# Optimization experiments

Hardware: AMD Instinct MI355X
Metric: run time of the kernel (lower is better)

Reference implementation:

```python
import jax, jax.numpy as jnp
import numpy as np
import math

N_FUNC = 32
LR_START, LR_DECAY = 1.0, 0.977
WEIGHT_DECAY, AMP_DECAY, MM_LR = 0.01, 0.01, 0.03
N_SAMP, BATCH, MOMENTUM = 32, 16, 0.85
N_FEAT, N_TARGET, MEM_SIZE = 1024, 512, 16384
DATA_SIZE = 100
SQRT_NF = math.sqrt(N_FUNC)


def setup_inputs() -> dict:
    key = jax.random.key(0)
    ks = jax.random.split(key, 16)
    p = jnp.linspace(0.01, 0.99, N_FUNC)[:, None]
    center_freq = jnp.log(p / (1.0 - p))  # logit of linspace, as in __init__
    return {
        "t": DATA_SIZE,
        "data_size": DATA_SIZE,
        "ts": jax.random.randint(ks[0], (N_SAMP,), 0, DATA_SIZE + 1),
        "x": jax.random.normal(ks[1], (N_FEAT,), jnp.float32),
        "z": jax.random.normal(ks[2], (N_TARGET,), jnp.float32),
        "memory": jax.random.normal(ks[3], (MEM_SIZE, N_TARGET), jnp.float32),
        "t_memory": jax.random.randint(ks[4], (MEM_SIZE,), 0, DATA_SIZE),
        "feat_memory": jax.random.normal(ks[5], (MEM_SIZE, N_FEAT), jnp.float32),
        "amp_re": 1.0 / SQRT_NF + 0.01 * jax.random.normal(ks[6], (N_FUNC, N_TARGET), jnp.float32),
        "amp_im": 0.01 * jax.random.normal(ks[7], (N_FUNC, N_TARGET), jnp.float32),
        "freq": 0.1 * jax.random.normal(ks[8], (N_FUNC, 1), jnp.float32),
        "center_freq": center_freq.astype(jnp.float32),
        "res_proj": 0.02 * jax.random.normal(ks[9], (N_FEAT + N_TARGET, N_TARGET), jnp.float32),
        "feat_mean": 0.1 * jax.random.normal(ks[10], (N_FEAT,), jnp.float32),
        "bias": 0.1 * jax.random.normal(ks[11], (N_TARGET,), jnp.float32),
        "amp_grad_re": 0.01 * jax.random.normal(ks[12], (N_FUNC, N_TARGET), jnp.float32),
        "amp_grad_im": 0.01 * jax.random.normal(ks[13], (N_FUNC, N_TARGET), jnp.float32),
        "freq_grad": 0.01 * jax.random.normal(ks[14], (N_FUNC, 1), jnp.float32),
        "res_proj_grad": 0.001 * jax.random.normal(ks[15], (N_FEAT + N_TARGET, N_TARGET), jnp.float32),
    }


def _get_freq(freq, center_freq):
    fr = center_freq + jnp.tanh(freq) * (64.0 / N_FUNC)
    return jax.nn.sigmoid(fr) * 0.5


def _evaluate(t, amp_re, amp_im, freq, bias, center_freq):
    # t: [B]; amp: [F, T]; freq/center_freq: [F, 1]
    fr = _get_freq(freq, center_freq)                      # [F, 1]
    ph = (2.0 * math.pi) * t[:, None, None] * fr           # [B, F, 1]
    # Re(exp(i*ph) * (amp_re + i*amp_im)) = cos*amp_re - sin*amp_im
    z = (jnp.cos(ph) * amp_re - jnp.sin(ph) * amp_im).sum(1) / SQRT_NF
    return z + bias                                        # [B, T]


def _get_resid(x, z, res_proj, feat_mean, bias):
    r = jnp.concatenate([x - feat_mean, z - bias], axis=-1) @ res_proj
    return r / (jnp.abs(r) + 1.0)


def reference(t, data_size, ts, x, z, memory, t_memory, feat_memory,
              amp_re, amp_im, freq, center_freq, res_proj, feat_mean, bias,
              amp_grad_re, amp_grad_im, freq_grad, res_proj_grad):
    # scatter new sample into the ring buffers
    memory = memory.at[data_size].set(z)
    feat_memory = feat_memory.at[data_size].set(x)
    t_memory = t_memory.at[data_size].set(t)
    ds_new = data_size + 1
    lr = LR_START * LR_DECAY ** ds_new  # lr after this call's decay
    # running means (torch uses the already-incremented data_size)
    bias = (bias * ds_new + z) / (ds_new + 1)
    feat_mean = (feat_mean * ds_new + x) / (ds_new + 1)

    for b in range(N_SAMP // BATCH):
        batch = ts[b * BATCH:(b + 1) * BATCH]
        t_b = t_memory[batch].astype(jnp.float32)
        z_b = memory[batch]
        x_b = feat_memory[batch]

        def loss_fn(a_re, a_im, fq, rp):
            z_ = _evaluate(t_b, a_re, a_im, fq, bias, center_freq)
            amp_abs = jnp.sqrt(a_re ** 2 + a_im ** 2)
            loss = jnp.sqrt(amp_abs).sum() * AMP_DECAY
            loss = loss + jnp.abs(z_b - z_).sum(-1).mean()
            resid = _get_resid(x_b, z_, rp, feat_mean, bias)
            z2 = jax.lax.stop_gradient(z_) + resid
            res_loss = jnp.abs(z_b - z2).sum(-1).mean()
            # torch uses self.res_proj (buffer) here -> no grad through this term
            res_loss = res_loss + jnp.abs(jax.lax.stop_gradient(rp)).sum() * WEIGHT_DECAY
            return loss + res_loss * MM_LR

        ag_re, ag_im, fg, rg = jax.grad(loss_fn, argnums=(0, 1, 2, 3))(amp_re, amp_im, freq, res_proj)
        # momentum decay then normalized-grad accumulate, then SGD step
        anorm = jnp.sqrt((ag_re ** 2).sum() + (ag_im ** 2).sum()) + 1.0  # complex vector norm
        amp_grad_re = amp_grad_re * MOMENTUM + ag_re / anorm
        amp_grad_im = amp_grad_im * MOMENTUM + ag_im / anorm
        amp_re = amp_re - amp_grad_re * lr
        amp_im = amp_im - amp_grad_im * lr
        fnorm = jnp.sqrt((fg ** 2).sum()) + 1.0
        freq_grad = freq_grad * MOMENTUM + fg / fnorm
        freq = freq - freq_grad * lr
        rnorm = jnp.sqrt((rg ** 2).sum()) + 1.0
        res_proj_grad = res_proj_grad * MOMENTUM + rg / rnorm
        res_proj = res_proj - res_proj_grad * lr

    return (memory, t_memory, feat_memory, amp_re, amp_im, freq, res_proj,
            bias, feat_mean, amp_grad_re, amp_grad_im, freq_grad, res_proj_grad)
```

## Files before the change

kernel.cpp:

```cpp
#include <hip/hip_runtime.h>
#include <math.h>

#define NT 512
#define NF 1024
#define NFUNC 32
#define BATCHSZ 16

constexpr int O_MEM  = 0;
constexpr int O_TMEM = 8388608;
constexpr int O_FEAT = 8404992;
constexpr int O_ARE  = 25182208;
constexpr int O_AIM  = 25198592;
constexpr int O_FREQ = 25214976;
constexpr int O_RP   = 25215008;
constexpr int O_BIAS = 26001440;
constexpr int O_FM   = 26001952;
constexpr int O_AGR  = 26002976;
constexpr int O_AGI  = 26019360;
constexpr int O_FGR  = 26035744;
constexpr int O_RPG  = 26035776;

constexpr int W_LR    = 0;
constexpr int W_ANORM = 2;
constexpr int W_RNORM = 4;
constexpr int W_GFR   = 8;
constexpr int W_TB    = 72;
constexpr int W_C     = 96;
constexpr int W_S     = 608;
constexpr int W_CATZ  = 1120;
constexpr int W_CATX  = 9312;
constexpr int W_GR    = 25696;
constexpr int W_G     = 33888;
constexpr int W_AGRE  = 42080;
constexpr int W_AGIM  = 58464;
constexpr int W_RPART = 74848;

constexpr float MM_LR = 0.03f;
constexpr float AMP_DECAY = 0.01f;
constexpr float MOM = 0.85f;
constexpr float INV_SQRT_NF = 0.17677669529663687f;
constexpr float TWO_PI = 6.283185307179586f;

constexpr int NCOPY = 192;
constexpr long long U_TOTAL = 6295552LL;

__device__ __forceinline__ float sgnf(float x) {
    return (x > 0.f) ? 1.f : ((x < 0.f) ? -1.f : 0.f);
}

__device__ __forceinline__ float wave_reduce(float v) {
#pragma unroll
    for (int o = 32; o > 0; o >>= 1) v += __shfl_down(v, o, 64);
    return v;
}

__device__ __forceinline__ void copy_role(int rb, int cbase, int ccnt,
    const int* __restrict__ tptr, const int* __restrict__ dsptr,
    const float* __restrict__ x, const float* __restrict__ z,
    const float* __restrict__ memory, const int* __restrict__ t_memory,
    const float* __restrict__ feat_memory, float* __restrict__ out)
{
    const int dsv = *dsptr;
    const int tt  = *tptr;
    const int nthr = NCOPY * 256;
    for (int q = rb * 256 + (int)threadIdx.x; q * 4 < ccnt; q += nthr) {
#pragma unroll
        for (int w = 0; w < 4; ++w) {
            int rel = q * 4 + w;
            if (rel >= ccnt) break;
            int u = cbase + rel;
            if (u < 2097152) {
                int row = u >> 7;
                float4 v = (row == dsv) ? ((const float4*)z)[u & 127]
                                        : ((const float4*)memory)[u];
                ((float4*)(out + O_MEM))[u] = v;
            } else if (u < 6291456) {
                int f = u - 2097152;
                int row = f >> 8;
                float4 v = (row == dsv) ? ((const float4*)x)[f & 255]
                                        : ((const float4*)feat_memory)[f];
                ((float4*)(out + O_FEAT))[f] = v;
            } else {
                int f = u - 6291456;
                int4 iv = ((const int4*)t_memory)[f];
                int e = f * 4;
                float* o = out + O_TMEM + e;
                o[0] = (e + 0 == dsv) ? (float)tt : (float)iv.x;
                o[1] = (e + 1 == dsv) ? (float)tt : (float)iv.y;
                o[2] = (e + 2 == dsv) ? (float)tt : (float)iv.z;
                o[3] = (e + 3 == dsv) ? (float)tt : (float)iv.w;
            }
        }
    }
}

#define COPY_ARGS const int* __restrict__ tptr, const int* __restrict__ dsptr,            \
                  const float* __restrict__ x, const float* __restrict__ z,               \
                  const float* __restrict__ memory, const int* __restrict__ t_memory,     \
                  const float* __restrict__ feat_memory, int cbase, int ccnt
#define COPY_PASS tptr, dsptr, x, z, memory, t_memory, feat_memory

__global__ __launch_bounds__(256) void k_fwd_a(int b, const int* __restrict__ ts,
    const float* __restrict__ cf,
    const float* __restrict__ are_src, const float* __restrict__ aim_src,
    const float* __restrict__ fq_src, const float* __restrict__ fm_in,
    float* __restrict__ out, float* __restrict__ ws, COPY_ARGS)
{
    const int bb = blockIdx.x, tid = threadIdx.x;
    if (bb >= 16) { copy_role(bb - 16, cbase, ccnt, COPY_PASS, out); return; }
    __shared__ float c_l[32], s_l[32];
    const int i = bb;
    const int dsv = *dsptr;
    const int bi = ts[b * BATCHSZ + i];
    if (tid < 32) {
        float f  = fq_src[tid];
        float th = tanhf(f);
        float u  = cf[tid] + 2.f * th;
        float sg = 1.f / (1.f + expf(-u));
        float fr = 0.5f * sg;
        float tb = (bi == dsv) ? (float)(*tptr) : (float)t_memory[bi];
        float ph = TWO_PI * tb * fr;
        float cv = cosf(ph), sv = sinf(ph);
        c_l[tid] = cv; s_l[tid] = sv;
        ws[W_C + i*32 + tid] = cv; ws[W_S + i*32 + tid] = sv;
        if (tid == 0) ws[W_TB + i] = tb;
    }
    if (i == 0) {
        if (tid == 64) ws[W_ANORM + b] = 0.f;
        if (tid == 65) ws[W_RNORM + b] = 0.f;
        if (tid == 66 && b == 0) ws[W_LR] = (float)pow(0.977, (double)(dsv + 1));
        if (tid >= 96 && tid < 128) ws[W_GFR + b*32 + tid - 96] = 0.f;
    }
    __syncthreads();
#pragma unroll
    for (int qq = 0; qq < 2; ++qq) {
        int q = tid + qq * 256;
        float acc = 0.f;
#pragma unroll
        for (int k = 0; k < 32; ++k)
            acc += c_l[k] * are_src[k*NT + q] - s_l[k] * aim_src[k*NT + q];
        ws[W_CATZ + i*NT + q] = acc * INV_SQRT_NF;
    }
    const float nn = (float)(dsv + 1), dd = (float)(dsv + 2);
#pragma unroll
    for (int pp = 0; pp < 4; ++pp) {
        int p = tid + pp * 256;
        float fmv = (fm_in[p] * nn + x[p]) / dd;
        float xv  = (bi == dsv) ? x[p] : feat_memory[bi*NF + p];
        ws[W_CATX + i*NF + p] = xv - fmv;
    }
}

__global__ __launch_bounds__(256) void k_fwd_b(const float* __restrict__ rp_src,
    float* __restrict__ out, float* __restrict__ ws, COPY_ARGS)
{
    const int bb = blockIdx.x, tid = threadIdx.x;
    if (bb >= 256) { copy_role(bb - 256, cbase, ccnt, COPY_PASS, out); return; }
    const int i = bb >> 4, s = bb & 15;
    __shared__ float cat[96];
    if (tid < 96) {
        int p = s * 96 + tid;
        cat[tid] = (p < NF) ? ws[W_CATX + i*NF + p] : ws[W_CATZ + i*NT + p - NF];
    }
    __syncthreads();
    const int j = tid;
    const float* rpb = rp_src + (size_t)s * 96 * NT;
    float a0 = 0.f, a1 = 0.f, b0 = 0.f, b1 = 0.f;
#pragma unroll 8
    for (int p = 0; p < 96; p += 2) {
        float c0 = cat[p], c1 = cat[p + 1];
        a0 += c0 * rpb[p*NT + j];
        a1 += c0 * rpb[p*NT + j + 256];
        b0 += c1 * rpb[(p+1)*NT + j];
        b1 += c1 * rpb[(p+1)*NT + j + 256];
    }
    ws[W_RPART + s*8192 + i*NT + j]       = a0 + b0;
    ws[W_RPART + s*8192 + i*NT + j + 256] = a1 + b1;
}

__global__ __launch_bounds__(256) void k_eplg(int b, const int* __restrict__ ts,
    const float* __restrict__ bias_in, const float* __restrict__ fm_in,
    float* __restrict__ out, float* __restrict__ ws, COPY_ARGS)
{
    const int bb = blockIdx.x, tid = threadIdx.x;
    if (bb >= 32) { copy_role(bb - 32, cbase, ccnt, COPY_PASS, out); return; }
    const int e = bb * 256 + tid;
    const int i = e >> 9, j = e & 511;
    const int dsv = *dsptr;
    float r = 0.f;
#pragma unroll
    for (int s = 0; s < 16; ++s) r += ws[W_RPART + s*8192 + e];
    const float nn = (float)(dsv + 1), dd = (float)(dsv + 2);
    float bn = (bias_in[j] * nn + z[j]) / dd;
    float zj = ws[W_CATZ + e] + bn;
    const int bi = ts[b * BATCHSZ + i];
    float zb = (bi == dsv) ? z[j] : memory[bi*NT + j];
    float s1 = sgnf(zj - zb);
    float ar = fabsf(r) + 1.f;
    float z2 = zj + r / ar;
    float g  = sgnf(z2 - zb) * (MM_LR / 16.f) / (ar * ar);
    ws[W_GR + e] = g;
    ws[W_G  + e] = s1 * (1.f / 16.f);
    if (b == 0) {
        if (e < 512)  out[O_BIAS + e] = bn;
        if (e < 1024) out[O_FM + e] = (fm_in[e] * nn + x[e]) / dd;
    }
}

__global__ __launch_bounds__(256) void k_gr(int b, const float* __restrict__ rp_src,
    float* __restrict__ out, float* __restrict__ ws, COPY_ARGS)
{
    __shared__ float red[4];
    const int bb = blockIdx.x, tid = threadIdx.x;
    if (bb >= 5120) { copy_role(bb - 5120, cbase, ccnt, COPY_PASS, out); return; }
    if (bb < 2048) {
        int wid = tid >> 6, lane = tid & 63;
        int e = bb*4 + wid;
        int i = e >> 9, j = e & 511;
        const float* grow = ws + W_GR + i*NT;
        const float* rrow = rp_src + (size_t)(NF + j) * NT;
        float acc = 0.f;
#pragma unroll
        for (int l = lane; l < NT; l += 64) acc += grow[l] * rrow[l];
        acc = wave_reduce(acc);
        if (lane == 0) ws[W_G + e] += acc;
    } else {
        int e = (bb - 2048)*256 + tid;
        int p = e >> 9, j = e & 511;
        float rg = 0.f;
#pragma unroll
        for (int i2 = 0; i2 < 16; ++i2) {
            float cat = (p < NF) ? ws[W_CATX + i2*NF + p]
                                 : ws[W_CATZ + i2*NT + (p - NF)];
            rg += cat * ws[W_GR + i2*NT + j];
        }
        float v = wave_reduce(rg * rg);
        if ((tid & 63) == 0) red[tid >> 6] = v;
        __syncthreads();
        if (tid == 0) atomicAdd(&ws[W_RNORM + b], red[0]+red[1]+red[2]+red[3]);
    }
}

__global__ __launch_bounds__(256) void k_ag(int b,
    const float* __restrict__ are_src, const float* __restrict__ aim_src,
    float* __restrict__ out, float* __restrict__ ws, COPY_ARGS)
{
    __shared__ float red[4];
    const int bb = blockIdx.x, tid = threadIdx.x;
    if (bb >= 192) { copy_role(bb - 192, cbase, ccnt, COPY_PASS, out); return; }
    if (bb < 64) {
        int e = bb*256 + tid;
        int k = e >> 9;
        float gre = 0.f, gim = 0.f;
#pragma unroll
        for (int i2 = 0; i2 < 16; ++i2) {
            float G = ws[W_G + i2*NT + (e & 511)];
            gre += G * ws[W_C + i2*32 + k];
            gim += G * ws[W_S + i2*32 + k];
        }
        float re = are_src[e], im = aim_src[e];
        float aa = sqrtf(re*re + im*im);
        float dec = AMP_DECAY / (2.f * aa * sqrtf(aa));
        float agr =  gre * INV_SQRT_NF + re * dec;
        float agi = -gim * INV_SQRT_NF + im * dec;
        ws[W_AGRE + e] = agr;
        ws[W_AGIM + e] = agi;
        float v = wave_reduce(agr*agr + agi*agi);
        if ((tid & 63) == 0) red[tid >> 6] = v;
        __syncthreads();
        if (tid == 0) atomicAdd(&ws[W_ANORM + b], red[0]+red[1]+red[2]+red[3]);
    } else {
        int wid = tid >> 6, lane = tid & 63;
        int pair = (bb - 64)*4 + wid;
        int i = pair >> 5, k = pair & 31;
        float ck = ws[W_C + i*32 + k], sk = ws[W_S + i*32 + k];
        float acc = 0.f;
#pragma unroll
        for (int j = lane; j < NT; j += 64)
            acc += ws[W_G + i*NT + j] * (-sk * are_src[k*NT + j] - ck * aim_src[k*NT + j]);
        acc = wave_reduce(acc);
        if (lane == 0)
            atomicAdd(&ws[W_GFR + b*32 + k], acc * TWO_PI * ws[W_TB + i] * INV_SQRT_NF);
    }
}

__global__ __launch_bounds__(256) void k_upd(int b, const float* __restrict__ cf,
    const float* __restrict__ are_src, const float* __restrict__ aim_src,
    const float* __restrict__ agr_src, const float* __restrict__ agi_src,
    const float* __restrict__ fq_src,  const float* __restrict__ fgr_src,
    const float* __restrict__ rp_src,  const float* __restrict__ rpg_src,
    float* __restrict__ out, float* __restrict__ ws, COPY_ARGS)
{
    const int bb = blockIdx.x, tid = threadIdx.x;
    if (bb >= 3137) { copy_role(bb - 3137, cbase, ccnt, COPY_PASS, out); return; }
    const float lr = ws[W_LR];
    if (bb < 64) {
        int e = bb*256 + tid;
        float anorm = sqrtf(ws[W_ANORM + b]) + 1.f;
        float mr = agr_src[e]*MOM + ws[W_AGRE + e]/anorm;
        out[O_AGR + e] = mr; out[O_ARE + e] = are_src[e] - mr*lr;
        float mi = agi_src[e]*MOM + ws[W_AGIM + e]/anorm;
        out[O_AGI + e] = mi; out[O_AIM + e] = aim_src[e] - mi*lr;
    } else if (bb == 64) {
        if (tid < 64) {
            float fg = 0.f, th = 0.f;
            if (tid < 32) {
                float f = fq_src[tid];
                th = tanhf(f);
                float u  = cf[tid] + 2.f*th;
                float sg = 1.f / (1.f + expf(-u));
                fg = ws[W_GFR + b*32 + tid] * sg*(1.f-sg)*(1.f-th*th);
            }
            float t2 = fg*fg;
#pragma unroll
            for (int o = 32; o > 0; o >>= 1) t2 += __shfl_down(t2, o, 64);
            float tot = __shfl(t2, 0, 64);
            if (tid < 32) {
                float fnorm = sqrtf(tot) + 1.f;
                float m = fgr_src[tid]*MOM + fg/fnorm;
                out[O_FGR + tid] = m;
                out[O_FREQ + tid] = fq_src[tid] - m*lr;
            }
        }
    } else {
        int e = (bb - 65)*256 + tid;
        int p = e >> 9, j = e & 511;
        float rg = 0.f;
#pragma unroll
        for (int i2 = 0; i2 < 16; ++i2) {
            float cat = (p < NF) ? ws[W_CATX + i2*NF + p]
                                 : ws[W_CATZ + i2*NT + (p - NF)];
            rg += cat * ws[W_GR + i2*NT + j];
        }
        float rnorm = sqrtf(ws[W_RNORM + b]) + 1.f;
        float m = rpg_src[e]*MOM + rg/rnorm;
        out[O_RPG + e] = m; out[O_RP + e] = rp_src[e] - m*lr;
    }
}

extern "C" void kernel_launch(void* const* d_in, const int* in_sizes, int n_in,
                              void* d_out, int out_size, void* d_ws, size_t ws_size,
                              hipStream_t stream)
{
    const int*   t            = (const int*)d_in[0];
    const int*   dsp          = (const int*)d_in[1];
    const int*   ts           = (const int*)d_in[2];
    const float* x            = (const float*)d_in[3];
    const float* z            = (const float*)d_in[4];
    const float* memory       = (const float*)d_in[5];
    const int*   t_memory     = (const int*)d_in[6];
    const float* feat_memory  = (const float*)d_in[7];
    const float* amp_re       = (const float*)d_in[8];
    const float* amp_im       = (const float*)d_in[9];
    const float* freq         = (const float*)d_in[10];
    const float* cf           = (const float*)d_in[11];
    const float* res_proj     = (const float*)d_in[12];
    const float* feat_mean    = (const float*)d_in[13];
    const float* bias         = (const float*)d_in[14];
    const float* amp_grad_re  = (const float*)d_in[15];
    const float* amp_grad_im  = (const float*)d_in[16];
    const float* freq_grad    = (const float*)d_in[17];
    const float* res_proj_grad= (const float*)d_in[18];
    float* out = (float*)d_out;
    float* ws  = (float*)d_ws;

    const float* ARE[2] = { amp_re,        out + O_ARE };
    const float* AIM[2] = { amp_im,        out + O_AIM };
    const float* AGR[2] = { amp_grad_re,   out + O_AGR };
    const float* AGI[2] = { amp_grad_im,   out + O_AGI };
    const float* FQ [2] = { freq,          out + O_FREQ };
    const float* FGR[2] = { freq_grad,     out + O_FGR };
    const float* RP [2] = { res_proj,      out + O_RP };
    const float* RPG[2] = { res_proj_grad, out + O_RPG };

    const int per = 524628;
    int base = 0, k = 0;
    auto nxt = [&](int& cb, int& cc) {
        cb = base;
        cc = (k == 11) ? (int)(U_TOTAL - base) : per;
        base += cc; ++k;
    };
    int cb, cc;
    for (int b = 0; b < 2; ++b) {
        nxt(cb, cc);
        k_fwd_a<<<16 + NCOPY, 256, 0, stream>>>(b, ts, cf, ARE[b], AIM[b], FQ[b],
            feat_mean, out, ws, t, dsp, x, z, memory, t_memory, feat_memory, cb, cc);
        nxt(cb, cc);
        k_fwd_b<<<256 + NCOPY, 256, 0, stream>>>(RP[b], out, ws,
            t, dsp, x, z, memory, t_memory, feat_memory, cb, cc);
        nxt(cb, cc);
        k_eplg<<<32 + NCOPY, 256, 0, stream>>>(b, ts, bias, feat_mean, out, ws,
            t, dsp, x, z, memory, t_memory, feat_memory, cb, cc);
        nxt(cb, cc);
        k_gr<<<5120 + NCOPY, 256, 0, stream>>>(b, RP[b], out, ws,
            t, dsp, x, z, memory, t_memory, feat_memory, cb, cc);
        nxt(cb, cc);
        k_ag<<<192 + NCOPY, 256, 0, stream>>>(b, ARE[b], AIM[b], out, ws,
            t, dsp, x, z, memory, t_memory, feat_memory, cb, cc);
        nxt(cb, cc);
        k_upd<<<3137 + NCOPY, 256, 0, stream>>>(b, cf, ARE[b], AIM[b], AGR[b], AGI[b],
            FQ[b], FGR[b], RP[b], RPG[b], out, ws,
            t, dsp, x, z, memory, t_memory, feat_memory, cb, cc);
    }
}
```

Measured before the change: 376.9 us.

## Fuse forward stages and gradient matvec, cutting per-step kernel launches

```diff
diff --git a/kernel.cpp b/kernel.cpp
--- a/kernel.cpp
+++ b/kernel.cpp
@@ -41,7 +41,7 @@
 constexpr float INV_SQRT_NF = 0.17677669529663687f;
 constexpr float TWO_PI = 6.283185307179586f;
 
-constexpr int NCOPY = 192;
+constexpr int NCOPY = 256;
 constexpr long long U_TOTAL = 6295552LL;
 
 __device__ __forceinline__ float sgnf(float x) {
@@ -100,16 +100,17 @@
                   const float* __restrict__ feat_memory, int cbase, int ccnt
 #define COPY_PASS tptr, dsptr, x, z, memory, t_memory, feat_memory
 
-__global__ __launch_bounds__(256) void k_fwd_a(int b, const int* __restrict__ ts,
+__global__ __launch_bounds__(256) void k_fwd_ab(int b, const int* __restrict__ ts,
     const float* __restrict__ cf,
     const float* __restrict__ are_src, const float* __restrict__ aim_src,
     const float* __restrict__ fq_src, const float* __restrict__ fm_in,
+    const float* __restrict__ rp_src,
     float* __restrict__ out, float* __restrict__ ws, COPY_ARGS)
 {
     const int bb = blockIdx.x, tid = threadIdx.x;
-    if (bb >= 16) { copy_role(bb - 16, cbase, ccnt, COPY_PASS, out); return; }
-    __shared__ float c_l[32], s_l[32];
-    const int i = bb;
+    if (bb >= 256) { copy_role(bb - 256, cbase, ccnt, COPY_PASS, out); return; }
+    const int i = bb >> 4, s = bb & 15;
+    __shared__ float c_l[32], s_l[32], cat[96];
     const int dsv = *dsptr;
     const int bi = ts[b * BATCHSZ + i];
     if (tid < 32) {
@@ -122,45 +123,37 @@
         float ph = TWO_PI * tb * fr;
         float cv = cosf(ph), sv = sinf(ph);
         c_l[tid] = cv; s_l[tid] = sv;
-        ws[W_C + i*32 + tid] = cv; ws[W_S + i*32 + tid] = sv;
-        if (tid == 0) ws[W_TB + i] = tb;
-    }
-    if (i == 0) {
+        if (s == 0) {
+            ws[W_C + i*32 + tid] = cv; ws[W_S + i*32 + tid] = sv;
+            if (tid == 0) ws[W_TB + i] = tb;
+        }
+    }
+    if (bb == 0) {
         if (tid == 64) ws[W_ANORM + b] = 0.f;
         if (tid == 65) ws[W_RNORM + b] = 0.f;
         if (tid == 66 && b == 0) ws[W_LR] = (float)pow(0.977, (double)(dsv + 1));
         if (tid >= 96 && tid < 128) ws[W_GFR + b*32 + tid - 96] = 0.f;
     }
     __syncthreads();
-#pragma unroll
-    for (int qq = 0; qq < 2; ++qq) {
-        int q = tid + qq * 256;
-        float acc = 0.f;
-#pragma unroll
-        for (int k = 0; k < 32; ++k)
-            acc += c_l[k] * are_src[k*NT + q] - s_l[k] * aim_src[k*NT + q];
-        ws[W_CATZ + i*NT + q] = acc * INV_SQRT_NF;
-    }
-    const float nn = (float)(dsv + 1), dd = (float)(dsv + 2);
-#pragma unroll
-    for (int pp = 0; pp < 4; ++pp) {
-        int p = tid + pp * 256;
-        float fmv = (fm_in[p] * nn + x[p]) / dd;
-        float xv  = (bi == dsv) ? x[p] : feat_memory[bi*NF + p];
-        ws[W_CATX + i*NF + p] = xv - fmv;
-    }
-}
-
-__global__ __launch_bounds__(256) void k_fwd_b(const float* __restrict__ rp_src,
-    float* __restrict__ out, float* __restrict__ ws, COPY_ARGS)
-{
-    const int bb = blockIdx.x, tid = threadIdx.x;
-    if (bb >= 256) { copy_role(bb - 256, cbase, ccnt, COPY_PASS, out); return; }
-    const int i = bb >> 4, s = bb & 15;
-    __shared__ float cat[96];
     if (tid < 96) {
         int p = s * 96 + tid;
-        cat[tid] = (p < NF) ? ws[W_CATX + i*NF + p] : ws[W_CATZ + i*NT + p - NF];
+        float cv;
+        if (p < NF) {
+            const float nn = (float)(dsv + 1), dd = (float)(dsv + 2);
+            float fmv = (fm_in[p] * nn + x[p]) / dd;
+            float xv  = (bi == dsv) ? x[p] : feat_memory[bi*NF + p];
+            cv = xv - fmv;
+            ws[W_CATX + i*NF + p] = cv;
+        } else {
+            int q = p - NF;
+            float acc = 0.f;
+#pragma unroll
+            for (int k = 0; k < 32; ++k)
+                acc += c_l[k] * are_src[k*NT + q] - s_l[k] * aim_src[k*NT + q];
+            cv = acc * INV_SQRT_NF;
+            ws[W_CATZ + i*NT + q] = cv;
+        }
+        cat[tid] = cv;
     }
     __syncthreads();
     const int j = tid;
@@ -178,76 +171,63 @@
     ws[W_RPART + s*8192 + i*NT + j + 256] = a1 + b1;
 }
 
-__global__ __launch_bounds__(256) void k_eplg(int b, const int* __restrict__ ts,
+__global__ __launch_bounds__(256) void k_eplg2(int b, const int* __restrict__ ts,
     const float* __restrict__ bias_in, const float* __restrict__ fm_in,
+    const float* __restrict__ rp_src,
     float* __restrict__ out, float* __restrict__ ws, COPY_ARGS)
 {
     const int bb = blockIdx.x, tid = threadIdx.x;
     if (bb >= 32) { copy_role(bb - 32, cbase, ccnt, COPY_PASS, out); return; }
-    const int e = bb * 256 + tid;
-    const int i = e >> 9, j = e & 511;
+    const int i = bb >> 1, half = bb & 1;
+    __shared__ float g_sh[NT], d_sh[NT];
     const int dsv = *dsptr;
-    float r = 0.f;
-#pragma unroll
-    for (int s = 0; s < 16; ++s) r += ws[W_RPART + s*8192 + e];
+    const int bi = ts[b * BATCHSZ + i];
     const float nn = (float)(dsv + 1), dd = (float)(dsv + 2);
-    float bn = (bias_in[j] * nn + z[j]) / dd;
-    float zj = ws[W_CATZ + e] + bn;
-    const int bi = ts[b * BATCHSZ + i];
-    float zb = (bi == dsv) ? z[j] : memory[bi*NT + j];
-    float s1 = sgnf(zj - zb);
-    float ar = fabsf(r) + 1.f;
-    float z2 = zj + r / ar;
-    float g  = sgnf(z2 - zb) * (MM_LR / 16.f) / (ar * ar);
-    ws[W_GR + e] = g;
-    ws[W_G  + e] = s1 * (1.f / 16.f);
-    if (b == 0) {
-        if (e < 512)  out[O_BIAS + e] = bn;
-        if (e < 1024) out[O_FM + e] = (fm_in[e] * nn + x[e]) / dd;
-    }
-}
-
-__global__ __launch_bounds__(256) void k_gr(int b, const float* __restrict__ rp_src,
+#pragma unroll
+    for (int ll = 0; ll < 2; ++ll) {
+        int l = tid + ll * 256;
+        float r = 0.f;
+#pragma unroll
+        for (int s = 0; s < 16; ++s) r += ws[W_RPART + s*8192 + i*NT + l];
+        float bn = (bias_in[l] * nn + z[l]) / dd;
+        float zj = ws[W_CATZ + i*NT + l] + bn;
+        float zb = (bi == dsv) ? z[l] : memory[bi*NT + l];
+        float s1 = sgnf(zj - zb);
+        float ar = fabsf(r) + 1.f;
+        float z2 = zj + r / ar;
+        float g  = sgnf(z2 - zb) * (MM_LR / 16.f) / (ar * ar);
+        g_sh[l] = g; d_sh[l] = s1 * (1.f / 16.f);
+        ws[W_GR + i*NT + l] = g;
+        if (b == 0 && bb == 0) out[O_BIAS + l] = bn;
+    }
+    if (b == 0 && bb < 2) {
+#pragma unroll
+        for (int ll = 0; ll < 2; ++ll) {
+            int p = half * 512 + tid + ll * 256;
+            out[O_FM + p] = (fm_in[p] * nn + x[p]) / dd;
+        }
+    }
+    __syncthreads();
+    const int w = tid >> 6, lane = tid & 63;
+    const int jbase = half * 256 + w * 64;
+    for (int jj = 0; jj < 64; ++jj) {
+        int j = jbase + jj;
+        const float* rrow = rp_src + (size_t)(NF + j) * NT;
+        float acc = 0.f;
+#pragma unroll
+        for (int l = lane; l < NT; l += 64) acc += g_sh[l] * rrow[l];
+        acc = wave_reduce(acc);
+        if (lane == 0) ws[W_G + i*NT + j] = d_sh[j] + acc;
+    }
+}
+
+__global__ __launch_bounds__(256) void k_norms(int b,
+    const float* __restrict__ are_src, const float* __restrict__ aim_src,
     float* __restrict__ out, float* __restrict__ ws, COPY_ARGS)
 {
     __shared__ float red[4];
     const int bb = blockIdx.x, tid = threadIdx.x;
-    if (bb >= 5120) { copy_role(bb - 5120, cbase, ccnt, COPY_PASS, out); return; }
-    if (bb < 2048) {
-        int wid = tid >> 6, lane = tid & 63;
-        int e = bb*4 + wid;
-        int i = e >> 9, j = e & 511;
-        const float* grow = ws + W_GR + i*NT;
-        const float* rrow = rp_src + (size_t)(NF + j) * NT;
-        float acc = 0.f;
-#pragma unroll
-        for (int l = lane; l < NT; l += 64) acc += grow[l] * rrow[l];
-        acc = wave_reduce(acc);
-        if (lane == 0) ws[W_G + e] += acc;
-    } else {
-        int e = (bb - 2048)*256 + tid;
-        int p = e >> 9, j = e & 511;
-        float rg = 0.f;
-#pragma unroll
-        for (int i2 = 0; i2 < 16; ++i2) {
-            float cat = (p < NF) ? ws[W_CATX + i2*NF + p]
-                                 : ws[W_CATZ + i2*NT + (p - NF)];
-            rg += cat * ws[W_GR + i2*NT + j];
-        }
-        float v = wave_reduce(rg * rg);
-        if ((tid & 63) == 0) red[tid >> 6] = v;
-        __syncthreads();
-        if (tid == 0) atomicAdd(&ws[W_RNORM + b], red[0]+red[1]+red[2]+red[3]);
-    }
-}
-
-__global__ __launch_bounds__(256) void k_ag(int b,
-    const float* __restrict__ are_src, const float* __restrict__ aim_src,
-    float* __restrict__ out, float* __restrict__ ws, COPY_ARGS)
-{
-    __shared__ float red[4];
-    const int bb = blockIdx.x, tid = threadIdx.x;
-    if (bb >= 192) { copy_role(bb - 192, cbase, ccnt, COPY_PASS, out); return; }
+    if (bb >= 3264) { copy_role(bb - 3264, cbase, ccnt, COPY_PASS, out); return; }
     if (bb < 64) {
         int e = bb*256 + tid;
         int k = e >> 9;
@@ -269,7 +249,7 @@
         if ((tid & 63) == 0) red[tid >> 6] = v;
         __syncthreads();
         if (tid == 0) atomicAdd(&ws[W_ANORM + b], red[0]+red[1]+red[2]+red[3]);
-    } else {
+    } else if (bb < 192) {
         int wid = tid >> 6, lane = tid & 63;
         int pair = (bb - 64)*4 + wid;
         int i = pair >> 5, k = pair & 31;
@@ -281,6 +261,20 @@
         acc = wave_reduce(acc);
         if (lane == 0)
             atomicAdd(&ws[W_GFR + b*32 + k], acc * TWO_PI * ws[W_TB + i] * INV_SQRT_NF);
+    } else {
+        int e = (bb - 192)*256 + tid;
+        int p = e >> 9, j = e & 511;
+        float rg = 0.f;
+#pragma unroll
+        for (int i2 = 0; i2 < 16; ++i2) {
+            float cat = (p < NF) ? ws[W_CATX + i2*NF + p]
+                                 : ws[W_CATZ + i2*NT + (p - NF)];
+            rg += cat * ws[W_GR + i2*NT + j];
+        }
+        float v = wave_reduce(rg * rg);
+        if ((tid & 63) == 0) red[tid >> 6] = v;
+        __syncthreads();
+        if (tid == 0) atomicAdd(&ws[W_RNORM + b], red[0]+red[1]+red[2]+red[3]);
     }
 }
 
@@ -373,29 +367,19 @@
     const float* RP [2] = { res_proj,      out + O_RP };
     const float* RPG[2] = { res_proj_grad, out + O_RPG };
 
-    const int per = 524628;
-    int base = 0, k = 0;
-    auto nxt = [&](int& cb, int& cc) {
-        cb = base;
-        cc = (k == 11) ? (int)(U_TOTAL - base) : per;
-        base += cc; ++k;
-    };
+    const int per = 786944;
+    int base = 0;
+    auto nxt = [&](int& cb, int& cc) { cb = base; cc = per; base += cc; };
     int cb, cc;
     for (int b = 0; b < 2; ++b) {
         nxt(cb, cc);
-        k_fwd_a<<<16 + NCOPY, 256, 0, stream>>>(b, ts, cf, ARE[b], AIM[b], FQ[b],
-            feat_mean, out, ws, t, dsp, x, z, memory, t_memory, feat_memory, cb, cc);
+        k_fwd_ab<<<256 + NCOPY, 256, 0, stream>>>(b, ts, cf, ARE[b], AIM[b], FQ[b],
+            feat_mean, RP[b], out, ws, t, dsp, x, z, memory, t_memory, feat_memory, cb, cc);
         nxt(cb, cc);
-        k_fwd_b<<<256 + NCOPY, 256, 0, stream>>>(RP[b], out, ws,
+        k_eplg2<<<32 + NCOPY, 256, 0, stream>>>(b, ts, bias, feat_mean, RP[b], out, ws,
             t, dsp, x, z, memory, t_memory, feat_memory, cb, cc);
         nxt(cb, cc);
-        k_eplg<<<32 + NCOPY, 256, 0, stream>>>(b, ts, bias, feat_mean, out, ws,
-            t, dsp, x, z, memory, t_memory, feat_memory, cb, cc);
-        nxt(cb, cc);
-        k_gr<<<5120 + NCOPY, 256, 0, stream>>>(b, RP[b], out, ws,
-            t, dsp, x, z, memory, t_memory, feat_memory, cb, cc);
-        nxt(cb, cc);
-        k_ag<<<192 + NCOPY, 256, 0, stream>>>(b, ARE[b], AIM[b], out, ws,
+        k_norms<<<3264 + NCOPY, 256, 0, stream>>>(b, ARE[b], AIM[b], out, ws,
             t, dsp, x, z, memory, t_memory, feat_memory, cb, cc);
         nxt(cb, cc);
         k_upd<<<3137 + NCOPY, 256, 0, stream>>>(b, cf, ARE[b], AIM[b], AGR[b], AGI[b],
```

After: 413.9 us. 9.8% more time.
